# Kernel optimization log

Measured on AMD Instinct MI355X. Metric: run time of the kernel, lower is better.

The kernel has to match this reference:

```python
import jax, jax.numpy as jnp
import numpy as np


def setup_inputs() -> dict:
    key = jax.random.key(0)
    kx, ks = jax.random.split(key)
    M, N, D = 8192, 8192, 512
    X = jax.random.normal(kx, (M, D), dtype=jnp.float32)
    svs = jax.random.normal(ks, (N, D), dtype=jnp.float32)
    # scale = 1/(2*sigma^2); a plausible fitted value for standard-normal data
    scale = jnp.asarray(0.01, dtype=jnp.float32)
    return {"X": X, "svs": svs, "scale": scale}


def reference(X, svs, scale):
    N, D = svs.shape
    x2 = jnp.sum(X * X, axis=-1, keepdims=True)          # [M, 1]
    s2 = jnp.sum(svs * svs, axis=-1)                      # [N]
    dist2 = x2 + s2[None, :] - 2.0 * (X @ svs.T)          # [M, N]
    dist2 = jnp.maximum(dist2, 0.0)
    log_p = (jax.scipy.special.logsumexp(-scale * dist2, axis=-1)
             - jnp.log(jnp.asarray(N, dtype=X.dtype))
             + (D / 2) * jnp.log(scale / jnp.pi))
    return log_p
```

## Files before the change

kernel.cpp:

```cpp
#include <hip/hip_runtime.h>
#include <hip/hip_bf16.h>
#include <hip/hip_fp8.h>
#include <math.h>

typedef __attribute__((ext_vector_type(4))) int   int4v;
typedef __attribute__((ext_vector_type(8))) int   int8v;
typedef __attribute__((ext_vector_type(4))) float f32x4;

#define BM 128
#define BN 128
#define BK 128

union frag_u { int8v v; int4v h[2]; };

__global__ __launch_bounds__(256) void prep_kernel(
    const float* __restrict__ X, const float* __restrict__ S,
    unsigned char* __restrict__ Xq, unsigned char* __restrict__ Sq,
    float* __restrict__ x2, float* __restrict__ s2,
    float* __restrict__ rowsum, int M, int R, int Dv)
{
    const int gid  = blockIdx.x * 256 + threadIdx.x;
    const int nthr = gridDim.x * 256;

    for (int i = gid; i < M; i += nthr) rowsum[i] = 0.f;

    const int lane = threadIdx.x & 63;
    const int wid  = gid >> 6;
    const int nw   = nthr >> 6;

    for (int row = wid; row < R; row += nw) {
        const float* rp;
        unsigned char* op;
        float* sq;
        if (row < M) { rp = X + (size_t)row * Dv;       op = Xq + (size_t)row * Dv;       sq = x2 + row; }
        else         { rp = S + (size_t)(row - M) * Dv; op = Sq + (size_t)(row - M) * Dv; sq = s2 + (row - M); }

        float acc = 0.f;
        for (int k = lane * 8; k < Dv; k += 64 * 8) {
            float4 v0 = *(const float4*)(rp + k);
            float4 v1 = *(const float4*)(rp + k + 4);
            acc += v0.x * v0.x + v0.y * v0.y + v0.z * v0.z + v0.w * v0.w;
            acc += v1.x * v1.x + v1.y * v1.y + v1.z * v1.z + v1.w * v1.w;
            int lo = __builtin_amdgcn_cvt_pk_fp8_f32(v0.x, v0.y, 0, false);
            lo     = __builtin_amdgcn_cvt_pk_fp8_f32(v0.z, v0.w, lo, true);
            int hi = __builtin_amdgcn_cvt_pk_fp8_f32(v1.x, v1.y, 0, false);
            hi     = __builtin_amdgcn_cvt_pk_fp8_f32(v1.z, v1.w, hi, true);
            union { int i2[2]; uint2 u; } pk;
            pk.i2[0] = lo; pk.i2[1] = hi;
            *(uint2*)(op + k) = pk.u;
        }
#pragma unroll
        for (int off = 1; off < 64; off <<= 1)
            acc += __shfl_xor(acc, off, 64);
        if (lane == 0) *sq = acc;
    }
}

template<int DVC>
__global__ __launch_bounds__(256, 2) void kde_gemm_kernel(
    const unsigned char* __restrict__ Xq,
    const unsigned char* __restrict__ Sq,
    const float* __restrict__ x2,
    const float* __restrict__ s2,
    const float* __restrict__ scale_p,
    float* __restrict__ rowsum,
    int M, int N, int Dv)
{
    const int D  = DVC ? DVC : Dv;
    const int NT = D / BK;

    __shared__ char smem[65536];

    const int tid  = threadIdx.x;
    const int wave = tid >> 6;
    const int lane = tid & 63;
    const int quad = lane >> 4;
    const int l16  = lane & 15;

    const int m0 = blockIdx.x * BM;
    const int n0 = blockIdx.y * BN;
    const int wm = (wave & 1) * 64;
    const int wn = (wave >> 1) * 64;

    const float sc = *scale_p;

    f32x4 acc[4][4] = {};

    const int srow0 = wave * 8 + (lane >> 3);
    const int cg    = (lane & 7) ^ (lane >> 3);
    const unsigned char* gA = Xq + (size_t)(m0 + srow0) * D + cg * 16;
    const unsigned char* gB = Sq + (size_t)(n0 + srow0) * D + cg * 16;

    auto stage = [&](int slab, int bufo) {
        const size_t ko = (size_t)slab * BK;
#pragma unroll
        for (int rd = 0; rd < 4; ++rd) {
            __builtin_amdgcn_global_load_lds(
                (const __attribute__((address_space(1))) void*)(gA + (size_t)rd * 32 * D + ko),
                (__attribute__((address_space(3))) void*)(smem + bufo + rd * 4096 + wave * 1024),
                16, 0, 0);
            __builtin_amdgcn_global_load_lds(
                (const __attribute__((address_space(1))) void*)(gB + (size_t)rd * 32 * D + ko),
                (__attribute__((address_space(3))) void*)(smem + bufo + 16384 + rd * 4096 + wave * 1024),
                16, 0, 0);
        }
    };

    stage(0, 0);
    if (NT > 1) stage(1, 32768);

    const int e     = l16 & 7;
    const int offLo = ((2 * quad)     ^ e) * 16;
    const int offHi = ((2 * quad + 1) ^ e) * 16;
    int aOff[4], bOff[4];
#pragma unroll
    for (int i = 0; i < 4; ++i) {
        aOff[i] = (wm + i * 16 + l16) * 128;
        bOff[i] = 16384 + (wn + i * 16 + l16) * 128;
    }

#pragma unroll
    for (int t = 0; t < NT; ++t) {
        if (t + 1 < NT) asm volatile("s_waitcnt vmcnt(8)" ::: "memory");
        else            asm volatile("s_waitcnt vmcnt(0)" ::: "memory");
        __builtin_amdgcn_s_barrier();

        const int bufo = (t & 1) * 32768;
        frag_u a_frag[4], b_frag[4];
#pragma unroll
        for (int mi = 0; mi < 4; ++mi) {
            a_frag[mi].h[0] = *(const int4v*)(smem + bufo + aOff[mi] + offLo);
            a_frag[mi].h[1] = *(const int4v*)(smem + bufo + aOff[mi] + offHi);
        }
#pragma unroll
        for (int ni = 0; ni < 4; ++ni) {
            b_frag[ni].h[0] = *(const int4v*)(smem + bufo + bOff[ni] + offLo);
            b_frag[ni].h[1] = *(const int4v*)(smem + bufo + bOff[ni] + offHi);
        }

        if (t + 2 < NT) {
            asm volatile("s_waitcnt lgkmcnt(0)" ::: "memory");
            __builtin_amdgcn_sched_barrier(0);
            __builtin_amdgcn_s_barrier();
            stage(t + 2, bufo);
        }

#pragma unroll
        for (int mi = 0; mi < 4; ++mi)
#pragma unroll
            for (int ni = 0; ni < 4; ++ni)
                acc[mi][ni] = __builtin_amdgcn_mfma_scale_f32_16x16x128_f8f6f4(
                    a_frag[mi].v, b_frag[ni].v, acc[mi][ni],
                    0, 0,
                    0, 0x7F7F7F7F,
                    0, 0x7F7F7F7F);
    }

    __syncthreads();
    float* wred = (float*)smem + wave * (64 * 20);

    float s2v[4];
#pragma unroll
    for (int ni = 0; ni < 4; ++ni)
        s2v[ni] = s2[n0 + wn + ni * 16 + l16];

#pragma unroll
    for (int mi = 0; mi < 4; ++mi) {
#pragma unroll
        for (int r = 0; r < 4; ++r) {
            const int rowL = mi * 16 + quad * 4 + r;
            const float xv = x2[m0 + wm + rowL];
            float sum = 0.f;
#pragma unroll
            for (int ni = 0; ni < 4; ++ni) {
                float d2 = xv + s2v[ni] - 2.0f * acc[mi][ni][r];
                d2 = fmaxf(d2, 0.f);
                sum += __expf(-sc * d2);
            }
            wred[rowL * 20 + l16] = sum;
        }
    }
    __syncthreads();

    float4 p0 = *(float4*)(wred + lane * 20 + 0);
    float4 p1 = *(float4*)(wred + lane * 20 + 4);
    float4 p2 = *(float4*)(wred + lane * 20 + 8);
    float4 p3 = *(float4*)(wred + lane * 20 + 12);
    float s = (p0.x + p0.y + p0.z + p0.w) + (p1.x + p1.y + p1.z + p1.w)
            + (p2.x + p2.y + p2.z + p2.w) + (p3.x + p3.y + p3.z + p3.w);
    atomicAdd(&rowsum[m0 + wm + lane], s);
}

__global__ void finalize_kernel(const float* __restrict__ rowsum,
                                const float* __restrict__ scale_p,
                                float* __restrict__ out, int M, int N, int Dv) {
    const int m = blockIdx.x * 256 + threadIdx.x;
    if (m < M) {
        const float sc = *scale_p;
        const float cst = -logf((float)N) + 0.5f * (float)Dv * logf(sc / 3.14159265358979f);
        out[m] = logf(rowsum[m]) + cst;
    }
}

extern "C" void kernel_launch(void* const* d_in, const int* in_sizes, int n_in,
                              void* d_out, int out_size, void* d_ws, size_t ws_size,
                              hipStream_t stream) {
    const float* X       = (const float*)d_in[0];
    const float* S       = (const float*)d_in[1];
    const float* scale_p = (const float*)d_in[2];
    float* out = (float*)d_out;

    const int M  = out_size;
    const int Dv = in_sizes[0] / M;
    const int N  = in_sizes[1] / Dv;

    char* ws = (char*)d_ws;
    unsigned char* Xq = (unsigned char*)ws;
    unsigned char* Sq = (unsigned char*)(ws + (size_t)M * Dv);
    float* x2     = (float*)(ws + (size_t)M * Dv + (size_t)N * Dv);
    float* s2     = x2 + M;
    float* rowsum = s2 + N;

    prep_kernel<<<2048, 256, 0, stream>>>(X, S, Xq, Sq, x2, s2, rowsum, M, M + N, Dv);

    dim3 grid(M / BM, N / BN);
    if (Dv == 512)
        kde_gemm_kernel<512><<<grid, 256, 0, stream>>>(Xq, Sq, x2, s2, scale_p, rowsum, M, N, Dv);
    else
        kde_gemm_kernel<0><<<grid, 256, 0, stream>>>(Xq, Sq, x2, s2, scale_p, rowsum, M, N, Dv);

    finalize_kernel<<<(M + 255) / 256, 256, 0, stream>>>(rowsum, scale_p, out, M, N, Dv);
}
```

Measured before the change: 122.3 us.

## Load B fragments directly from global into registers, halving LDS staging

```diff
diff --git a/kernel.cpp b/kernel.cpp
--- a/kernel.cpp
+++ b/kernel.cpp
@@ -69,7 +69,7 @@
     const int D  = DVC ? DVC : Dv;
     const int NT = D / BK;
 
-    __shared__ char smem[65536];
+    __shared__ char smem[32768];
 
     const int tid  = threadIdx.x;
     const int wave = tid >> 6;
@@ -89,71 +89,81 @@
     const int srow0 = wave * 8 + (lane >> 3);
     const int cg    = (lane & 7) ^ (lane >> 3);
     const unsigned char* gA = Xq + (size_t)(m0 + srow0) * D + cg * 16;
-    const unsigned char* gB = Sq + (size_t)(n0 + srow0) * D + cg * 16;
-
-    auto stage = [&](int slab, int bufo) {
+
+    auto stageA = [&](int slab, int bufo) {
         const size_t ko = (size_t)slab * BK;
 #pragma unroll
-        for (int rd = 0; rd < 4; ++rd) {
+        for (int rd = 0; rd < 4; ++rd)
             __builtin_amdgcn_global_load_lds(
                 (const __attribute__((address_space(1))) void*)(gA + (size_t)rd * 32 * D + ko),
                 (__attribute__((address_space(3))) void*)(smem + bufo + rd * 4096 + wave * 1024),
                 16, 0, 0);
-            __builtin_amdgcn_global_load_lds(
-                (const __attribute__((address_space(1))) void*)(gB + (size_t)rd * 32 * D + ko),
-                (__attribute__((address_space(3))) void*)(smem + bufo + 16384 + rd * 4096 + wave * 1024),
-                16, 0, 0);
-        }
     };
 
-    stage(0, 0);
-    if (NT > 1) stage(1, 32768);
+    const unsigned char* gBr = Sq + (size_t)(n0 + wn + l16) * D + quad * 32;
+    frag_u bfr[2][4];
+
+    auto loadB = [&](int slab, int p) {
+#pragma unroll
+        for (int ni = 0; ni < 4; ++ni) {
+            bfr[p][ni].h[0] = *(const int4v*)(gBr + (size_t)ni * 16 * D + (size_t)slab * BK);
+            bfr[p][ni].h[1] = *(const int4v*)(gBr + (size_t)ni * 16 * D + (size_t)slab * BK + 16);
+        }
+    };
+
+    stageA(0, 0);
+    loadB(0, 0);
+    if (NT > 1) stageA(1, 16384);
 
     const int e     = l16 & 7;
     const int offLo = ((2 * quad)     ^ e) * 16;
     const int offHi = ((2 * quad + 1) ^ e) * 16;
-    int aOff[4], bOff[4];
-#pragma unroll
-    for (int i = 0; i < 4; ++i) {
+    int aOff[4];
+#pragma unroll
+    for (int i = 0; i < 4; ++i)
         aOff[i] = (wm + i * 16 + l16) * 128;
-        bOff[i] = 16384 + (wn + i * 16 + l16) * 128;
-    }
 
 #pragma unroll
     for (int t = 0; t < NT; ++t) {
-        if (t + 1 < NT) asm volatile("s_waitcnt vmcnt(8)" ::: "memory");
-        else            asm volatile("s_waitcnt vmcnt(0)" ::: "memory");
+        if (t == 0) {
+            if (NT > 1) asm volatile("s_waitcnt vmcnt(4)" ::: "memory");
+            else        asm volatile("s_waitcnt vmcnt(0)" ::: "memory");
+        } else if (t == NT - 1) {
+            asm volatile("s_waitcnt vmcnt(8)" ::: "memory");
+        } else {
+            asm volatile("s_waitcnt vmcnt(12)" ::: "memory");
+        }
         __builtin_amdgcn_s_barrier();
 
-        const int bufo = (t & 1) * 32768;
-        frag_u a_frag[4], b_frag[4];
+        const int bufo = (t & 1) * 16384;
+        frag_u a_frag[4];
 #pragma unroll
         for (int mi = 0; mi < 4; ++mi) {
             a_frag[mi].h[0] = *(const int4v*)(smem + bufo + aOff[mi] + offLo);
             a_frag[mi].h[1] = *(const int4v*)(smem + bufo + aOff[mi] + offHi);
         }
-#pragma unroll
-        for (int ni = 0; ni < 4; ++ni) {
-            b_frag[ni].h[0] = *(const int4v*)(smem + bufo + bOff[ni] + offLo);
-            b_frag[ni].h[1] = *(const int4v*)(smem + bufo + bOff[ni] + offHi);
-        }
+
+        if (t + 1 < NT) loadB(t + 1, (t + 1) & 1);
 
         if (t + 2 < NT) {
             asm volatile("s_waitcnt lgkmcnt(0)" ::: "memory");
             __builtin_amdgcn_sched_barrier(0);
             __builtin_amdgcn_s_barrier();
-            stage(t + 2, bufo);
-        }
-
+            stageA(t + 2, bufo);
+        }
+
+        const int p = t & 1;
+        __builtin_amdgcn_s_setprio(1);
 #pragma unroll
         for (int mi = 0; mi < 4; ++mi)
 #pragma unroll
             for (int ni = 0; ni < 4; ++ni)
                 acc[mi][ni] = __builtin_amdgcn_mfma_scale_f32_16x16x128_f8f6f4(
-                    a_frag[mi].v, b_frag[ni].v, acc[mi][ni],
+                    a_frag[mi].v, bfr[p][ni].v, acc[mi][ni],
                     0, 0,
                     0, 0x7F7F7F7F,
                     0, 0x7F7F7F7F);
+        __builtin_amdgcn_s_setprio(0);
     }
 
     __syncthreads();
```

Measured after the change: 157.9 us. 1.29x slower.
